# Performance work log

Measured on AMD Instinct MI355X. Metric: run time of the kernel, lower is better.

The kernel has to match this reference:

```python
import jax, jax.numpy as jnp
import numpy as np

BULK, TOWER, E8D = 2048, 512, 8
NUM_LEVELS = 8  # training_levels
LN_EPS = 1e-6
RMS_EPS = 1e-6


def _layernorm(x, g, b, eps=LN_EPS):
    mu = jnp.mean(x, axis=-1, keepdims=True)
    var = jnp.mean((x - mu) ** 2, axis=-1, keepdims=True)
    return (x - mu) * jax.lax.rsqrt(var + eps) * g + b


def _rmsnorm(x, scale, eps=RMS_EPS):
    rms = jnp.sqrt(jnp.mean(x ** 2, axis=-1, keepdims=True) + eps)
    return x / rms * scale


def _nearest_d8(x):
    # Nearest point in D8 (integer vectors with even coordinate sum).
    f = jnp.round(x)
    err = x - f
    parity_odd = jnp.mod(jnp.sum(f, axis=-1), 2.0) != 0
    idx = jnp.argmax(jnp.abs(err), axis=-1)
    oh = jax.nn.one_hot(idx, E8D, dtype=x.dtype)
    worst_err = jnp.take_along_axis(err, idx[..., None], axis=-1)
    adj = jnp.where(worst_err >= 0, 1.0, -1.0)
    f_fix = f + oh * adj  # flip rounding of worst coordinate to restore even parity
    return jnp.where(parity_odd[..., None], f_fix, f)


def _nearest_e8(x):
    # E8 = D8 U (D8 + 1/2); pick the closer candidate.
    a = _nearest_d8(x)
    b = _nearest_d8(x - 0.5) + 0.5
    da = jnp.sum((x - a) ** 2, axis=-1)
    db = jnp.sum((x - b) ** 2, axis=-1)
    return jnp.where((da <= db)[..., None], a, b)


def _residual_e8_quantize(x, num_levels=NUM_LEVELS):
    # Residual VQ: per-level nearest E8 lattice point, subtract, accumulate.
    r = x
    q = jnp.zeros_like(x)
    for _ in range(num_levels):
        ql = _nearest_e8(r)
        q = q + ql
        r = r - ql
    return q


def setup_inputs() -> dict:
    key = jax.random.key(0)
    ks = jax.random.split(key, 8)
    B, S = 8, 2048
    s_bt = 1.0 / np.sqrt(BULK)
    s_t = 1.0 / np.sqrt(TOWER)
    s_e = 1.0 / np.sqrt(E8D)
    return {
        'x': jax.random.normal(ks[0], (B, S, BULK), dtype=jnp.float32),
        'W_bt': jax.random.uniform(ks[1], (BULK, TOWER), jnp.float32, -s_bt, s_bt),
        'b_bt': jnp.zeros((TOWER,), jnp.float32),
        'ln_et_g': jnp.ones((TOWER,), jnp.float32),
        'ln_et_b': jnp.zeros((TOWER,), jnp.float32),
        'W_t8': jax.random.uniform(ks[2], (TOWER, E8D), jnp.float32, -s_t, s_t),
        'b_t8': jnp.zeros((E8D,), jnp.float32),
        'rms_g': jnp.ones((E8D,), jnp.float32),
        'W_8t': jax.random.uniform(ks[3], (E8D, TOWER), jnp.float32, -s_e, s_e),
        'b_8t': jnp.zeros((TOWER,), jnp.float32),
        'ln_dt_g': jnp.ones((TOWER,), jnp.float32),
        'ln_dt_b': jnp.zeros((TOWER,), jnp.float32),
        'W_tb': jax.random.uniform(ks[4], (TOWER, BULK), jnp.float32, -s_t, s_t),
        'b_tb': jnp.zeros((BULK,), jnp.float32),
        'ln_db_g': jnp.ones((BULK,), jnp.float32),
        'ln_db_b': jnp.zeros((BULK,), jnp.float32),
    }


def reference(x, W_bt, b_bt, ln_et_g, ln_et_b, W_t8, b_t8, rms_g,
              W_8t, b_8t, ln_dt_g, ln_dt_b, W_tb, b_tb, ln_db_g, ln_db_b):
    B, S, D = x.shape
    h = x.reshape(B * S, D)
    # encode: bulk -> tower -> 8D continuous
    tower = _layernorm(h @ W_bt + b_bt, ln_et_g, ln_et_b)
    e8 = _rmsnorm(tower @ W_t8 + b_t8, rms_g)
    # residual E8 lattice quantization with straight-through estimator
    q = _residual_e8_quantize(e8, NUM_LEVELS)
    e8_q = e8 + jax.lax.stop_gradient(q - e8)
    # decode: 8D -> tower -> bulk
    t2 = _layernorm(e8_q @ W_8t + b_8t, ln_dt_g, ln_dt_b)
    out = _layernorm(t2 @ W_tb + b_tb, ln_db_g, ln_db_b)
    return out.reshape(B, S, D)
```

## Files before the change

### kernel.cpp

```cpp
#include <hip/hip_runtime.h>

#define BULK 2048
#define TOWER 512
#define E8D 8
#define NROWS 16384
#define LO_SCALE 2048.0f
#define LO_INV (1.0f / 2048.0f)

typedef _Float16 f16x8 __attribute__((ext_vector_type(8)));
typedef float f32x4 __attribute__((ext_vector_type(4)));

__global__ void k_conv_transpose(const float* __restrict__ in, int K, int N,
                                 _Float16* __restrict__ out_hi,
                                 _Float16* __restrict__ out_lo) {
    __shared__ float tile[32][33];
    int tx = threadIdx.x & 31, ty = threadIdx.x >> 5;
    int k0 = blockIdx.x * 32, n0 = blockIdx.y * 32;
#pragma unroll
    for (int i = 0; i < 32; i += 8)
        tile[ty + i][tx] = in[(size_t)(k0 + ty + i) * N + (n0 + tx)];
    __syncthreads();
#pragma unroll
    for (int i = 0; i < 32; i += 8) {
        int n = n0 + ty + i, k = k0 + tx;
        float v = tile[tx][ty + i];
        _Float16 h = (_Float16)v;
        _Float16 l = (_Float16)((v - (float)h) * LO_SCALE);
        out_hi[(size_t)n * K + k] = h;
        out_lo[(size_t)n * K + k] = l;
    }
}

template <bool A_FP32>
__global__ __launch_bounds__(256, 2) void k_gemm_split(
    const float* __restrict__ Af, const _Float16* __restrict__ Ah,
    const _Float16* __restrict__ Al, const _Float16* __restrict__ Bh,
    const _Float16* __restrict__ Bl, float* __restrict__ C, int K, int N) {
    __shared__ _Float16 lds[4][128][40];
    const int t = threadIdx.x;
    const int m0 = blockIdx.x * 128, n0 = blockIdx.y * 128;
    const int wid = t >> 6, lane = t & 63;
    const int wr = wid >> 1, wc = wid & 1;
    const int lr = lane & 15, kg = lane >> 4;

    f32x4 acc1[4][4] = {};
    f32x4 acc2[4][4] = {};

    const int sr = t >> 1;
    const int sc = (t & 1) * 16;

    for (int k0 = 0; k0 < K; k0 += 32) {
        __syncthreads();
        if constexpr (A_FP32) {
            const float* src = Af + (size_t)(m0 + sr) * K + k0 + sc;
            float arr[16];
            *(float4*)&arr[0]  = *(const float4*)(src + 0);
            *(float4*)&arr[4]  = *(const float4*)(src + 4);
            *(float4*)&arr[8]  = *(const float4*)(src + 8);
            *(float4*)&arr[12] = *(const float4*)(src + 12);
            f16x8 hv0, hv1, lv0, lv1;
#pragma unroll
            for (int e = 0; e < 8; ++e) {
                float va = arr[e], vb = arr[8 + e];
                _Float16 ha = (_Float16)va, hb = (_Float16)vb;
                hv0[e] = ha;
                hv1[e] = hb;
                lv0[e] = (_Float16)((va - (float)ha) * LO_SCALE);
                lv1[e] = (_Float16)((vb - (float)hb) * LO_SCALE);
            }
            *(f16x8*)&lds[0][sr][sc]     = hv0;
            *(f16x8*)&lds[0][sr][sc + 8] = hv1;
            *(f16x8*)&lds[1][sr][sc]     = lv0;
            *(f16x8*)&lds[1][sr][sc + 8] = lv1;
        } else {
            const _Float16* sah = Ah + (size_t)(m0 + sr) * K + k0 + sc;
            const _Float16* sal = Al + (size_t)(m0 + sr) * K + k0 + sc;
            *(f16x8*)&lds[0][sr][sc]     = *(const f16x8*)(sah);
            *(f16x8*)&lds[0][sr][sc + 8] = *(const f16x8*)(sah + 8);
            *(f16x8*)&lds[1][sr][sc]     = *(const f16x8*)(sal);
            *(f16x8*)&lds[1][sr][sc + 8] = *(const f16x8*)(sal + 8);
        }
        {
            const _Float16* sbh = Bh + (size_t)(n0 + sr) * K + k0 + sc;
            const _Float16* sbl = Bl + (size_t)(n0 + sr) * K + k0 + sc;
            *(f16x8*)&lds[2][sr][sc]     = *(const f16x8*)(sbh);
            *(f16x8*)&lds[2][sr][sc + 8] = *(const f16x8*)(sbh + 8);
            *(f16x8*)&lds[3][sr][sc]     = *(const f16x8*)(sbl);
            *(f16x8*)&lds[3][sr][sc + 8] = *(const f16x8*)(sbl + 8);
        }
        __syncthreads();

        f16x8 a_h[4], a_l[4], b_h[4], b_l[4];
#pragma unroll
        for (int m = 0; m < 4; ++m) {
            int r = wr * 64 + m * 16 + lr;
            a_h[m] = *(const f16x8*)&lds[0][r][kg * 8];
            a_l[m] = *(const f16x8*)&lds[1][r][kg * 8];
        }
#pragma unroll
        for (int n = 0; n < 4; ++n) {
            int r = wc * 64 + n * 16 + lr;
            b_h[n] = *(const f16x8*)&lds[2][r][kg * 8];
            b_l[n] = *(const f16x8*)&lds[3][r][kg * 8];
        }
#pragma unroll
        for (int m = 0; m < 4; ++m)
#pragma unroll
            for (int n = 0; n < 4; ++n) {
                acc1[m][n] = __builtin_amdgcn_mfma_f32_16x16x32_f16(
                    a_h[m], b_h[n], acc1[m][n], 0, 0, 0);
                acc2[m][n] = __builtin_amdgcn_mfma_f32_16x16x32_f16(
                    a_h[m], b_l[n], acc2[m][n], 0, 0, 0);
                acc2[m][n] = __builtin_amdgcn_mfma_f32_16x16x32_f16(
                    a_l[m], b_h[n], acc2[m][n], 0, 0, 0);
            }
    }

#pragma unroll
    for (int m = 0; m < 4; ++m)
#pragma unroll
        for (int n = 0; n < 4; ++n)
#pragma unroll
            for (int i = 0; i < 4; ++i) {
                int row = m0 + wr * 64 + m * 16 + kg * 4 + i;
                int col = n0 + wc * 64 + n * 16 + lr;
                C[(size_t)row * N + col] = acc1[m][n][i] + acc2[m][n][i] * LO_INV;
            }
}

__device__ inline void nearest_d8(const float* x, float* f) {
    float s = 0.f;
#pragma unroll
    for (int j = 0; j < 8; ++j) {
        f[j] = rintf(x[j]);
        s += f[j];
    }
    float besta = -1.f, beste = 0.f;
    int bidx = 0;
#pragma unroll
    for (int j = 0; j < 8; ++j) {
        float e = x[j] - f[j];
        float a = fabsf(e);
        if (a > besta) { besta = a; beste = e; bidx = j; }
    }
    if (fmodf(s, 2.0f) != 0.0f) {
        float adj = (beste >= 0.f) ? 1.f : -1.f;
#pragma unroll
        for (int j = 0; j < 8; ++j) f[j] += (j == bidx) ? adj : 0.f;
    }
}

__device__ inline void nearest_e8(const float* x, float* out) {
    float fa[8], xs[8], fb[8];
    nearest_d8(x, fa);
#pragma unroll
    for (int j = 0; j < 8; ++j) xs[j] = x[j] - 0.5f;
    nearest_d8(xs, fb);
#pragma unroll
    for (int j = 0; j < 8; ++j) fb[j] += 0.5f;
    float da = 0.f, db = 0.f;
#pragma unroll
    for (int j = 0; j < 8; ++j) {
        float ea = x[j] - fa[j], eb = x[j] - fb[j];
        da += ea * ea;
        db += eb * eb;
    }
    bool pa = (da <= db);
#pragma unroll
    for (int j = 0; j < 8; ++j) out[j] = pa ? fa[j] : fb[j];
}

__device__ inline float wred64(float v) {
#pragma unroll
    for (int off = 1; off < 64; off <<= 1) v += __shfl_xor(v, off, 64);
    return v;
}

__global__ __launch_bounds__(256) void k_rows(
    const float* __restrict__ pre1, const float* __restrict__ b_bt,
    const float* __restrict__ g_et, const float* __restrict__ be_et,
    const float* __restrict__ W_t8, const float* __restrict__ b_t8,
    const float* __restrict__ rms_g, const float* __restrict__ W_8t,
    const float* __restrict__ b_8t, const float* __restrict__ g_dt,
    const float* __restrict__ b_dt, _Float16* __restrict__ t2h,
    _Float16* __restrict__ t2l) {
    int wid = threadIdx.x >> 6, lane = threadIdx.x & 63;
    int row = blockIdx.x * 4 + wid;
    int cb = lane * 8;

    const float* src = pre1 + (size_t)row * TOWER + cb;
    float v[8];
    *(float4*)&v[0] = *(const float4*)(src);
    *(float4*)&v[4] = *(const float4*)(src + 4);
#pragma unroll
    for (int i = 0; i < 8; ++i) v[i] += b_bt[cb + i];

    float s = 0.f;
#pragma unroll
    for (int i = 0; i < 8; ++i) s += v[i];
    s = wred64(s);
    float mu = s * (1.f / 512.f);
    float ss = 0.f;
#pragma unroll
    for (int i = 0; i < 8; ++i) { float d = v[i] - mu; ss += d * d; }
    ss = wred64(ss);
    float inv = 1.f / sqrtf(ss * (1.f / 512.f) + 1e-6f);
    float tw[8];
#pragma unroll
    for (int i = 0; i < 8; ++i)
        tw[i] = (v[i] - mu) * inv * g_et[cb + i] + be_et[cb + i];

    float p[8] = {0.f, 0.f, 0.f, 0.f, 0.f, 0.f, 0.f, 0.f};
#pragma unroll
    for (int i = 0; i < 8; ++i) {
        const float* wr_ = W_t8 + (size_t)(cb + i) * 8;
#pragma unroll
        for (int j = 0; j < 8; ++j) p[j] += tw[i] * wr_[j];
    }
#pragma unroll
    for (int j = 0; j < 8; ++j) p[j] = wred64(p[j]);

    float e8[8];
    float ms = 0.f;
#pragma unroll
    for (int j = 0; j < 8; ++j) {
        e8[j] = p[j] + b_t8[j];
        ms += e8[j] * e8[j];
    }
    float rms = sqrtf(ms * (1.f / 8.f) + 1e-6f);
#pragma unroll
    for (int j = 0; j < 8; ++j) e8[j] = e8[j] / rms * rms_g[j];

    float q[8] = {0.f, 0.f, 0.f, 0.f, 0.f, 0.f, 0.f, 0.f};
    float r[8];
#pragma unroll
    for (int j = 0; j < 8; ++j) r[j] = e8[j];
#pragma unroll
    for (int lvl = 0; lvl < 8; ++lvl) {
        float ql[8];
        nearest_e8(r, ql);
#pragma unroll
        for (int j = 0; j < 8; ++j) { q[j] += ql[j]; r[j] -= ql[j]; }
    }

    float o[8];
#pragma unroll
    for (int i = 0; i < 8; ++i) {
        int c = cb + i;
        float acc = b_8t[c];
#pragma unroll
        for (int j = 0; j < 8; ++j) acc += q[j] * W_8t[(size_t)j * TOWER + c];
        o[i] = acc;
    }
    float s2 = 0.f;
#pragma unroll
    for (int i = 0; i < 8; ++i) s2 += o[i];
    s2 = wred64(s2);
    float mu2 = s2 * (1.f / 512.f);
    float ss2 = 0.f;
#pragma unroll
    for (int i = 0; i < 8; ++i) { float d = o[i] - mu2; ss2 += d * d; }
    ss2 = wred64(ss2);
    float inv2 = 1.f / sqrtf(ss2 * (1.f / 512.f) + 1e-6f);

    f16x8 hv, lv;
#pragma unroll
    for (int i = 0; i < 8; ++i) {
        int c = cb + i;
        float t2v = (o[i] - mu2) * inv2 * g_dt[c] + b_dt[c];
        _Float16 h = (_Float16)t2v;
        hv[i] = h;
        lv[i] = (_Float16)((t2v - (float)h) * LO_SCALE);
    }
    *(f16x8*)(t2h + (size_t)row * TOWER + cb) = hv;
    *(f16x8*)(t2l + (size_t)row * TOWER + cb) = lv;
}

__global__ __launch_bounds__(256) void k_ln2(float* __restrict__ out,
                                             const float* __restrict__ b_tb,
                                             const float* __restrict__ g,
                                             const float* __restrict__ b) {
    __shared__ float red[4];
    int t = threadIdx.x, wid = t >> 6, lane = t & 63;
    size_t base = (size_t)blockIdx.x * BULK;
    int cb = t * 8;
    float v[8];
    *(float4*)&v[0] = *(const float4*)(out + base + cb);
    *(float4*)&v[4] = *(const float4*)(out + base + cb + 4);
#pragma unroll
    for (int i = 0; i < 8; ++i) v[i] += b_tb[cb + i];

    float s = 0.f;
#pragma unroll
    for (int i = 0; i < 8; ++i) s += v[i];
    s = wred64(s);
    if (lane == 0) red[wid] = s;
    __syncthreads();
    float tot = red[0] + red[1] + red[2] + red[3];
    float mu = tot * (1.f / 2048.f);
    __syncthreads();
    float ss = 0.f;
#pragma unroll
    for (int i = 0; i < 8; ++i) { float d = v[i] - mu; ss += d * d; }
    ss = wred64(ss);
    if (lane == 0) red[wid] = ss;
    __syncthreads();
    float vtot = red[0] + red[1] + red[2] + red[3];
    float inv = 1.f / sqrtf(vtot * (1.f / 2048.f) + 1e-6f);
#pragma unroll
    for (int i = 0; i < 8; ++i) v[i] = (v[i] - mu) * inv * g[cb + i] + b[cb + i];
    *(float4*)(out + base + cb) = *(float4*)&v[0];
    *(float4*)(out + base + cb + 4) = *(float4*)&v[4];
}

extern "C" void kernel_launch(void* const* d_in, const int* in_sizes, int n_in,
                              void* d_out, int out_size, void* d_ws,
                              size_t ws_size, hipStream_t stream) {
    const float* x     = (const float*)d_in[0];
    const float* W_bt  = (const float*)d_in[1];
    const float* b_bt  = (const float*)d_in[2];
    const float* g_et  = (const float*)d_in[3];
    const float* be_et = (const float*)d_in[4];
    const float* W_t8  = (const float*)d_in[5];
    const float* b_t8  = (const float*)d_in[6];
    const float* rms_g = (const float*)d_in[7];
    const float* W_8t  = (const float*)d_in[8];
    const float* b_8t  = (const float*)d_in[9];
    const float* g_dt  = (const float*)d_in[10];
    const float* b_dt  = (const float*)d_in[11];
    const float* W_tb  = (const float*)d_in[12];
    const float* b_tb  = (const float*)d_in[13];
    const float* g_db  = (const float*)d_in[14];
    const float* b_db  = (const float*)d_in[15];
    float* out = (float*)d_out;

    char* w = (char*)d_ws;
    _Float16* Wbt_h = (_Float16*)w; w += (size_t)BULK * TOWER * 2;
    _Float16* Wbt_l = (_Float16*)w; w += (size_t)BULK * TOWER * 2;
    _Float16* Wtb_h = (_Float16*)w; w += (size_t)TOWER * BULK * 2;
    _Float16* Wtb_l = (_Float16*)w; w += (size_t)TOWER * BULK * 2;
    _Float16* t2h   = (_Float16*)w; w += (size_t)NROWS * TOWER * 2;
    _Float16* t2l   = (_Float16*)w; w += (size_t)NROWS * TOWER * 2;
    float* pre1 = out;

    k_conv_transpose<<<dim3(BULK / 32, TOWER / 32), 256, 0, stream>>>(
        W_bt, BULK, TOWER, Wbt_h, Wbt_l);
    k_conv_transpose<<<dim3(TOWER / 32, BULK / 32), 256, 0, stream>>>(
        W_tb, TOWER, BULK, Wtb_h, Wtb_l);

    k_gemm_split<true><<<dim3(NROWS / 128, TOWER / 128), 256, 0, stream>>>(
        x, nullptr, nullptr, Wbt_h, Wbt_l, pre1, BULK, TOWER);

    k_rows<<<NROWS / 4, 256, 0, stream>>>(pre1, b_bt, g_et, be_et, W_t8, b_t8,
                                          rms_g, W_8t, b_8t, g_dt, b_dt, t2h,
                                          t2l);

    k_gemm_split<false><<<dim3(NROWS / 128, BULK / 128), 256, 0, stream>>>(
        nullptr, t2h, t2l, Wtb_h, Wtb_l, out, TOWER, BULK);

    k_ln2<<<NROWS, 256, 0, stream>>>(out, b_tb, g_db, b_db);
}
```

Before: 564.6 us.

## Double-buffer GEMM tiles in LDS using direct global-to-LDS async loads

Rewrites the split-fp16 GEMM main loop to use two LDS buffers, so the next K-tile is prefetched while MFMAs run on the current one. The fp16 B operands, and A when it is fp16, are staged with global_load_lds (direct global-to-LDS) instead of going through registers. fp32 A is loaded into registers early and converted and written to LDS after the MFMAs. The padding removal (row stride 40 to 32) may add LDS bank conflicts on the fragment reads, and the extra buffer doubles LDS use, which may limit occupancy.

```diff
diff --git a/kernel.cpp b/kernel.cpp
--- a/kernel.cpp
+++ b/kernel.cpp
@@ -9,6 +9,11 @@
 
 typedef _Float16 f16x8 __attribute__((ext_vector_type(8)));
 typedef float f32x4 __attribute__((ext_vector_type(4)));
+
+#define GLOAD(g, l)                                                        \
+    __builtin_amdgcn_global_load_lds(                                      \
+        (const __attribute__((address_space(1))) void*)(g),                \
+        (__attribute__((address_space(3))) void*)(l), 16, 0, 0)
 
 __global__ void k_conv_transpose(const float* __restrict__ in, int K, int N,
                                  _Float16* __restrict__ out_hi,
@@ -36,7 +41,7 @@
     const float* __restrict__ Af, const _Float16* __restrict__ Ah,
     const _Float16* __restrict__ Al, const _Float16* __restrict__ Bh,
     const _Float16* __restrict__ Bl, float* __restrict__ C, int K, int N) {
-    __shared__ _Float16 lds[4][128][40];
+    __shared__ _Float16 lds[2][4][128][32];
     const int t = threadIdx.x;
     const int m0 = blockIdx.x * 128, n0 = blockIdx.y * 128;
     const int wid = t >> 6, lane = t & 63;
@@ -46,62 +51,88 @@
     f32x4 acc1[4][4] = {};
     f32x4 acc2[4][4] = {};
 
-    const int sr = t >> 1;
-    const int sc = (t & 1) * 16;
-
-    for (int k0 = 0; k0 < K; k0 += 32) {
-        __syncthreads();
-        if constexpr (A_FP32) {
-            const float* src = Af + (size_t)(m0 + sr) * K + k0 + sc;
-            float arr[16];
-            *(float4*)&arr[0]  = *(const float4*)(src + 0);
-            *(float4*)&arr[4]  = *(const float4*)(src + 4);
-            *(float4*)&arr[8]  = *(const float4*)(src + 8);
-            *(float4*)&arr[12] = *(const float4*)(src + 12);
-            f16x8 hv0, hv1, lv0, lv1;
-#pragma unroll
-            for (int e = 0; e < 8; ++e) {
-                float va = arr[e], vb = arr[8 + e];
-                _Float16 ha = (_Float16)va, hb = (_Float16)vb;
-                hv0[e] = ha;
-                hv1[e] = hb;
-                lv0[e] = (_Float16)((va - (float)ha) * LO_SCALE);
-                lv1[e] = (_Float16)((vb - (float)hb) * LO_SCALE);
+    const int sr = t >> 1, sc = (t & 1) * 16;
+    const float* aptr = A_FP32 ? (Af + (size_t)(m0 + sr) * K + sc) : nullptr;
+    float areg[16];
+
+    const int c0 = wid * 2;
+    const _Float16* bhp =
+        Bh + (size_t)(n0 + c0 * 16 + (lane >> 2)) * K + (lane & 3) * 8;
+    const _Float16* blp =
+        Bl + (size_t)(n0 + c0 * 16 + (lane >> 2)) * K + (lane & 3) * 8;
+
+    const _Float16* gop = (wid == 0) ? Ah : (wid == 1) ? Al : (wid == 2) ? Bh : Bl;
+    const int r0 = ((wid < 2) ? m0 : n0) + (lane >> 2);
+    const _Float16* gp = A_FP32 ? nullptr : (gop + (size_t)r0 * K + (lane & 3) * 8);
+
+    auto loadA = [&](int k0) {
+        const float* p = aptr + k0;
+        *(float4*)&areg[0] = *(const float4*)(p);
+        *(float4*)&areg[4] = *(const float4*)(p + 4);
+        *(float4*)&areg[8] = *(const float4*)(p + 8);
+        *(float4*)&areg[12] = *(const float4*)(p + 12);
+    };
+    auto stageB = [&](int k0, int bb) {
+        GLOAD(bhp + k0, &lds[bb][2][c0 * 16][0]);
+        GLOAD(bhp + k0 + (size_t)16 * K, &lds[bb][2][c0 * 16 + 16][0]);
+        GLOAD(blp + k0, &lds[bb][3][c0 * 16][0]);
+        GLOAD(blp + k0 + (size_t)16 * K, &lds[bb][3][c0 * 16 + 16][0]);
+    };
+    auto writeA = [&](int bb) {
+        f16x8 hv0, hv1, lv0, lv1;
+#pragma unroll
+        for (int e = 0; e < 8; ++e) {
+            float va = areg[e], vb = areg[8 + e];
+            _Float16 ha = (_Float16)va, hb = (_Float16)vb;
+            hv0[e] = ha;
+            hv1[e] = hb;
+            lv0[e] = (_Float16)((va - (float)ha) * LO_SCALE);
+            lv1[e] = (_Float16)((vb - (float)hb) * LO_SCALE);
+        }
+        *(f16x8*)&lds[bb][0][sr][sc] = hv0;
+        *(f16x8*)&lds[bb][0][sr][sc + 8] = hv1;
+        *(f16x8*)&lds[bb][1][sr][sc] = lv0;
+        *(f16x8*)&lds[bb][1][sr][sc + 8] = lv1;
+    };
+    auto stageAll = [&](int k0, int bb) {
+#pragma unroll
+        for (int j = 0; j < 8; ++j)
+            GLOAD(gp + k0 + (size_t)(j * 16) * K, &lds[bb][wid][j * 16][0]);
+    };
+
+    if constexpr (A_FP32) {
+        loadA(0);
+        stageB(0, 0);
+        writeA(0);
+    } else {
+        stageAll(0, 0);
+    }
+    __syncthreads();
+
+    const int nk = K / 32;
+    for (int kt = 0; kt < nk; ++kt) {
+        const int b = kt & 1;
+        if (kt + 1 < nk) {
+            if constexpr (A_FP32) {
+                loadA((kt + 1) * 32);
+                stageB((kt + 1) * 32, b ^ 1);
+            } else {
+                stageAll((kt + 1) * 32, b ^ 1);
             }
-            *(f16x8*)&lds[0][sr][sc]     = hv0;
-            *(f16x8*)&lds[0][sr][sc + 8] = hv1;
-            *(f16x8*)&lds[1][sr][sc]     = lv0;
-            *(f16x8*)&lds[1][sr][sc + 8] = lv1;
-        } else {
-            const _Float16* sah = Ah + (size_t)(m0 + sr) * K + k0 + sc;
-            const _Float16* sal = Al + (size_t)(m0 + sr) * K + k0 + sc;
-            *(f16x8*)&lds[0][sr][sc]     = *(const f16x8*)(sah);
-            *(f16x8*)&lds[0][sr][sc + 8] = *(const f16x8*)(sah + 8);
-            *(f16x8*)&lds[1][sr][sc]     = *(const f16x8*)(sal);
-            *(f16x8*)&lds[1][sr][sc + 8] = *(const f16x8*)(sal + 8);
-        }
-        {
-            const _Float16* sbh = Bh + (size_t)(n0 + sr) * K + k0 + sc;
-            const _Float16* sbl = Bl + (size_t)(n0 + sr) * K + k0 + sc;
-            *(f16x8*)&lds[2][sr][sc]     = *(const f16x8*)(sbh);
-            *(f16x8*)&lds[2][sr][sc + 8] = *(const f16x8*)(sbh + 8);
-            *(f16x8*)&lds[3][sr][sc]     = *(const f16x8*)(sbl);
-            *(f16x8*)&lds[3][sr][sc + 8] = *(const f16x8*)(sbl + 8);
-        }
-        __syncthreads();
+        }
 
         f16x8 a_h[4], a_l[4], b_h[4], b_l[4];
 #pragma unroll
         for (int m = 0; m < 4; ++m) {
             int r = wr * 64 + m * 16 + lr;
-            a_h[m] = *(const f16x8*)&lds[0][r][kg * 8];
-            a_l[m] = *(const f16x8*)&lds[1][r][kg * 8];
+            a_h[m] = *(const f16x8*)&lds[b][0][r][kg * 8];
+            a_l[m] = *(const f16x8*)&lds[b][1][r][kg * 8];
         }
 #pragma unroll
         for (int n = 0; n < 4; ++n) {
             int r = wc * 64 + n * 16 + lr;
-            b_h[n] = *(const f16x8*)&lds[2][r][kg * 8];
-            b_l[n] = *(const f16x8*)&lds[3][r][kg * 8];
+            b_h[n] = *(const f16x8*)&lds[b][2][r][kg * 8];
+            b_l[n] = *(const f16x8*)&lds[b][3][r][kg * 8];
         }
 #pragma unroll
         for (int m = 0; m < 4; ++m)
@@ -114,6 +145,11 @@
                 acc2[m][n] = __builtin_amdgcn_mfma_f32_16x16x32_f16(
                     a_l[m], b_h[n], acc2[m][n], 0, 0, 0);
             }
+
+        if constexpr (A_FP32) {
+            if (kt + 1 < nk) writeA(b ^ 1);
+        }
+        __syncthreads();
     }
 
 #pragma unroll
```

Result: faster. 545.0 us (-3.5%).
